# Kernel optimization log

Hardware: AMD Instinct MI355X
Metric: run time of the kernel (lower is better)

## Reference

```python
import jax, jax.numpy as jnp
import numpy as np

# ---- static config (LCNN wirenet) ----
K = 128            # fixed junction count per type (n_dyn_junc // n_type)
N_PTS0 = 32
N_PTS1 = 8
SCALE = N_PTS0 // N_PTS1   # maxpool1d kernel/stride = 4
DIM_LOI = 128
DIM_FC = 1024
FEATURE_DIM = 8
USE_COOD = 0.0
USE_SLOP = 0.0
HW = 128
B = 2
# static u<v pair indices (torch: meshgrid -> c = u < v), P = K*(K-1)/2
IU_np, IV_np = np.triu_indices(K, k=1)
P = IU_np.shape[0]
IU = jnp.asarray(IU_np, jnp.int32)
IV = jnp.asarray(IV_np, jnp.int32)
LAMBDA = jnp.linspace(0.0, 1.0, N_PTS0)[:, None]  # [32,1]


def setup_inputs() -> dict:
    key = jax.random.key(0)
    ks = jax.random.split(key, 8)
    inputs = jax.random.normal(ks[0], (B, 5, HW, HW), jnp.float32)
    features = jax.random.normal(ks[1], (B, 256, HW, HW), jnp.float32)
    fc1_w = jax.random.normal(ks[2], (DIM_LOI, 256), jnp.float32) * 0.05
    fc1_b = jnp.zeros((DIM_LOI,), jnp.float32)
    d_in = DIM_LOI * N_PTS1 + FEATURE_DIM  # 1032
    w1 = jax.random.normal(ks[3], (d_in, DIM_FC), jnp.float32) * 0.03
    b1 = jnp.zeros((DIM_FC,), jnp.float32)
    w2 = jax.random.normal(ks[4], (DIM_FC, DIM_FC), jnp.float32) * 0.03
    b2 = jnp.zeros((DIM_FC,), jnp.float32)
    w3 = jax.random.normal(ks[5], (DIM_FC, 1), jnp.float32) * 0.03
    b3 = jnp.zeros((1,), jnp.float32)
    return dict(inputs=inputs, features=features, fc1_w=fc1_w, fc1_b=fc1_b,
                w1=w1, b1=b1, w2=w2, b2=b2, w3=w3, b3=b3)


def _nms(a):
    # a: [1,H,W]; 3x3 max-pool NMS, keep only local maxima
    ap = jax.lax.reduce_window(a, -jnp.inf, jax.lax.max, (1, 3, 3), (1, 1, 1), 'SAME')
    return a * (a == ap).astype(a.dtype)


def _sample_lines(jmap, joff):
    # jmap: [1,H,W], joff: [1,2,H,W]  (inference path: dummy junc/Lpos)
    n_type = 1
    jm = _nms(jmap).reshape(n_type, -1)            # [1, HW*HW]
    jo = joff.reshape(n_type, 2, -1)
    score, index = jax.lax.top_k(jm, K)            # [1,K]
    y = (index // HW).astype(jnp.float32) + jnp.take_along_axis(jo[:, 0], index, 1) + 0.5
    x = (index % HW).astype(jnp.float32) + jnp.take_along_axis(jo[:, 1], index, 1) + 0.5
    xy = jnp.stack([y, x], -1)                     # [1,K,2]
    # inference dummies: junc=zeros(1,2), jtyp=zeros(1), Lpos=zeros(2,2)
    junc = jnp.zeros((1, 2), jnp.float32)
    jtyp = jnp.zeros((1,), jnp.int32)
    dist = jnp.sum((xy[:, :, None, :] - junc) ** 2, -1)  # [1,K,1]
    cost = jnp.min(dist, -1)
    match = jnp.argmin(dist, -1).astype(jnp.int32)       # [1,K]
    Njunc = 1
    match = jnp.where(jtyp[match] != jnp.arange(n_type, dtype=jnp.int32)[:, None], Njunc, match)
    match = jnp.where(cost > 1.5 * 1.5, Njunc, match).reshape(-1)  # [K]
    up, vp = match[IU], match[IV]
    Lpos = jnp.zeros((2, 2), jnp.float32)
    label = Lpos[up, vp]                           # [P]
    xyf = xy.reshape(n_type * K, 2)
    xyu, xyv = xyf[IU], xyf[IV]                    # [P,2]
    u2v = xyu - xyv
    u2v = u2v / jnp.clip(jnp.sqrt(jnp.sum(u2v ** 2, -1, keepdims=True)), 1e-6)
    feat = jnp.concatenate([
        xyu / HW * USE_COOD, xyv / HW * USE_COOD, u2v * USE_SLOP,
        (IU[:, None] > K).astype(jnp.float32), (IV[:, None] > K).astype(jnp.float32)], 1)  # [P,8]
    line = jnp.stack([xyu, xyv], 1)                # [P,2,2]
    return line, label, feat


def _loi_pool(xfeat, line):
    # xfeat: [C,H,W], line: [P,2,2] -> [P,C,N_PTS1]
    p = line[:, 0:1, :] * LAMBDA + line[:, 1:2, :] * (1.0 - LAMBDA) - 0.5  # [P,32,2]
    p = p.reshape(-1, 2)
    px, py = p[:, 0], p[:, 1]
    px0 = jnp.clip(jnp.floor(px), 0, HW - 1)
    py0 = jnp.clip(jnp.floor(py), 0, HW - 1)
    px1 = jnp.clip(px0 + 1, 0, HW - 1)
    py1 = jnp.clip(py0 + 1, 0, HW - 1)
    px0l = px0.astype(jnp.int32); py0l = py0.astype(jnp.int32)
    px1l = px1.astype(jnp.int32); py1l = py1.astype(jnp.int32)
    xp = (xfeat[:, px0l, py0l] * (px1 - px) * (py1 - py)
          + xfeat[:, px1l, py0l] * (px - px0) * (py1 - py)
          + xfeat[:, px0l, py1l] * (px1 - px) * (py - py0)
          + xfeat[:, px1l, py1l] * (px - px0) * (py - py0))  # [C, P*32]
    xp = xp.reshape(DIM_LOI, -1, N_PTS0).transpose(1, 0, 2)  # [P,C,32]
    # MaxPool1d(kernel=4, stride=4)
    return xp.reshape(xp.shape[0], DIM_LOI, N_PTS1, SCALE).max(-1)  # [P,C,8]


def _forward(inputs, features, fc1_w, fc1_b, w1, b1, w2, b2, w3, b3):
    b, _, r, c = inputs.shape
    out = jnp.transpose(inputs, (1, 0, 2, 3))       # [5,B,H,W]
    jmap_logits = out[0:2].reshape(1, 2, b, r, c)
    joff_logits = out[3:5].reshape(1, 2, b, r, c)
    jmap = jax.nn.softmax(jnp.transpose(jmap_logits, (2, 0, 1, 3, 4)), axis=2)[:, :, 1]  # [B,1,H,W]
    joff = jax.nn.sigmoid(jnp.transpose(joff_logits, (2, 0, 1, 3, 4))) - 0.5             # [B,1,2,H,W]
    # fc1: 1x1 conv 256 -> dim_loi
    xf = jnp.einsum('bchw,dc->bdhw', features, fc1_w) + fc1_b[None, :, None, None]
    lines, labels, feats = jax.vmap(_sample_lines)(jmap, joff)   # [B,P,2,2],[B,P],[B,P,8]
    # sample_lines runs under torch.no_grad()
    lines = jax.lax.stop_gradient(lines)
    labels = jax.lax.stop_gradient(labels)
    feats = jax.lax.stop_gradient(feats)
    xp = jax.vmap(_loi_pool)(xf, lines)             # [B,P,C,8]
    xv = xp.reshape(-1, N_PTS1 * DIM_LOI)           # [B*P, 1024] (C-major then pts)
    xv = jnp.concatenate([xv, feats.reshape(-1, FEATURE_DIM)], 1)  # [B*P, 1032]
    h = jax.nn.relu(xv @ w1 + b1)
    h = jax.nn.relu(h @ w2 + b2)
    scores = (h @ w3 + b3).reshape(-1)              # [B*P]
    return scores, labels.reshape(-1), lines


def reference(inputs, features, fc1_w, fc1_b, w1, b1, w2, b2, w3, b3):
    return _forward(inputs, features, fc1_w, fc1_b, w1, b1, w2, b2, w3, b3)
```

## Files before the change

kernel.cpp:

```cpp
#include <hip/hip_runtime.h>
#include <hip/hip_bf16.h>
#include <math.h>

#define HW 128
#define NPIX 16384
#define KTOP 128
#define PPAIR 8128
#define NB 2
#define DIMLOI 128
#define NROWS (NB*PPAIR)
#define MPAD 16384

typedef __bf16 bf16x8 __attribute__((ext_vector_type(8)));
typedef __bf16 bf16x4 __attribute__((ext_vector_type(4)));
typedef float floatx4 __attribute__((ext_vector_type(4)));

__device__ __forceinline__ unsigned long long mk_key(float v, int idx) {
    return ((unsigned long long)__float_as_uint(v) << 32) |
           (unsigned long long)(0xFFFFFFFFu - (unsigned)idx);
}

__device__ __forceinline__ unsigned long long shfl_xor_u64(unsigned long long x, int m) {
    unsigned lo = (unsigned)x, hi = (unsigned)(x >> 32);
    lo = __shfl_xor(lo, m);
    hi = __shfl_xor(hi, m);
    return ((unsigned long long)hi << 32) | lo;
}

__device__ __forceinline__ void bitonic_stage(unsigned long long V[4], int lane, int j, int k) {
    if (j >= 64) {
        int qm = j >> 6;
        #pragma unroll
        for (int q = 0; q < 4; q++) {
            int p = q ^ qm;
            if (p > q) {
                int i = q * 64 + lane;
                bool desc = ((i & k) == 0);
                unsigned long long a = V[q], b = V[p];
                unsigned long long hi = a > b ? a : b, lo = a > b ? b : a;
                V[q] = desc ? hi : lo;
                V[p] = desc ? lo : hi;
            }
        }
    } else {
        #pragma unroll
        for (int q = 0; q < 4; q++) {
            int i = q * 64 + lane;
            unsigned long long p = shfl_xor_u64(V[q], j);
            bool lower = (lane & j) == 0;
            bool desc = ((i & k) == 0);
            bool keepmax = (desc == lower);
            unsigned long long mx = V[q] > p ? V[q] : p;
            unsigned long long mn = V[q] > p ? p : V[q];
            V[q] = keepmax ? mx : mn;
        }
    }
}

__device__ __forceinline__ void sort256_desc(unsigned long long V[4], int lane) {
    #pragma unroll
    for (int k = 2; k <= 256; k <<= 1)
        #pragma unroll
        for (int j = k >> 1; j >= 1; j >>= 1)
            bitonic_stage(V, lane, j, k);
}

__device__ __forceinline__ void merge256_desc(unsigned long long V[4], int lane) {
    #pragma unroll
    for (int j = 128; j >= 1; j >>= 1)
        bitonic_stage(V, lane, j, 256);
}

__global__ __launch_bounds__(256) void nms_sort_kernel(const float* __restrict__ inp,
                                                       unsigned long long* __restrict__ tkeys) {
    __shared__ float jm[10 * HW];
    __shared__ unsigned long long cand[256];
    __shared__ int scnt;
    int blk = blockIdx.x;
    int b   = blockIdx.y;
    int tid = threadIdx.x, lane = tid & 63;
    int r0  = blk * 8;
    int rlo = (r0 > 0) ? r0 - 1 : 0;
    int rhi = (r0 + 8 < HW) ? r0 + 8 : HW - 1;
    int nrows = rhi - rlo + 1;

    for (int i = tid; i < nrows * HW; i += 256) {
        int pix = rlo * HW + i;
        float l0 = inp[((long)b * 5 + 0) * NPIX + pix];
        float l1 = inp[((long)b * 5 + 1) * NPIX + pix];
        float m = fmaxf(l0, l1);
        float e0 = expf(l0 - m), e1 = expf(l1 - m);
        jm[i] = e1 / (e0 + e1);
    }
    cand[tid] = 0ull;
    if (tid == 0) scnt = 0;
    __syncthreads();

    #pragma unroll
    for (int i = 0; i < 4; i++) {
        int pl = i * 256 + tid;
        int r = r0 + (pl >> 7), c = pl & 127;
        float v = jm[(r - rlo) * HW + c];
        float m = v;
        for (int dr = -1; dr <= 1; dr++) {
            int rr = r + dr;
            if (rr < 0 || rr >= HW) continue;
            for (int dc = -1; dc <= 1; dc++) {
                int cc = c + dc;
                if (cc < 0 || cc >= HW) continue;
                m = fmaxf(m, jm[(rr - rlo) * HW + cc]);
            }
        }
        float nv = (v == m) ? v : 0.f;
        bool has = (nv > 0.f);
        unsigned long long mask = __ballot(has);
        int n = __popcll(mask);
        int wbase = 0;
        if (lane == 0 && n) wbase = atomicAdd(&scnt, n);
        wbase = __shfl(wbase, 0);
        if (has) {
            int pos = wbase + __popcll(mask & ((1ull << lane) - 1ull));
            if (pos < 256) cand[pos] = mk_key(nv, r * HW + c);
        }
    }
    __syncthreads();
    if (blk == 0 && tid < 128 && tid >= scnt) cand[tid] = mk_key(0.f, tid);
    __syncthreads();

    if (tid < 64) {
        unsigned long long V[4];
        #pragma unroll
        for (int q = 0; q < 4; q++) V[q] = cand[q * 64 + lane];
        sort256_desc(V, lane);
        #pragma unroll
        for (int q = 0; q < 2; q++)
            tkeys[((long)b * 16 + blk) * 128 + q * 64 + lane] = V[q];
    }
}

__global__ __launch_bounds__(512) void topk_merge_kernel(const unsigned long long* __restrict__ tkeys,
                                                         const float* __restrict__ inp,
                                                         float* __restrict__ xy) {
    __shared__ unsigned long long Lb[16 * 128];
    __shared__ unsigned long long Mb[8 * 128];
    int b = blockIdx.x;
    int tid = threadIdx.x, w = tid >> 6, lane = tid & 63;
    for (int i = tid; i < 16 * 128; i += 512) Lb[i] = tkeys[(long)b * 2048 + i];
    __syncthreads();

    unsigned long long* src = Lb;
    unsigned long long* dst = Mb;
    for (int nact = 8; nact >= 1; nact >>= 1) {
        unsigned long long V[4];
        if (w < nact) {
            #pragma unroll
            for (int q = 0; q < 2; q++) V[q] = src[(2 * w) * 128 + q * 64 + lane];
            #pragma unroll
            for (int q = 2; q < 4; q++) {
                int t = (q - 2) * 64 + lane;
                V[q] = src[(2 * w + 1) * 128 + 127 - t];
            }
            merge256_desc(V, lane);
        }
        __syncthreads();
        if (w < nact) {
            #pragma unroll
            for (int q = 0; q < 2; q++) dst[w * 128 + q * 64 + lane] = V[q];
        }
        __syncthreads();
        unsigned long long* tmp = src; src = dst; dst = tmp;
    }

    if (tid < KTOP) {
        unsigned long long key = src[tid];
        int wi = (int)(0xFFFFFFFFu - (unsigned)(key & 0xFFFFFFFFull));
        int row = wi >> 7, col = wi & 127;
        float l3 = inp[((long)b * 5 + 3) * NPIX + wi];
        float l4 = inp[((long)b * 5 + 4) * NPIX + wi];
        float joy = 1.f / (1.f + expf(-l3)) - 0.5f;
        float jox = 1.f / (1.f + expf(-l4)) - 0.5f;
        xy[(b * KTOP + tid) * 2 + 0] = (float)row + joy + 0.5f;
        xy[(b * KTOP + tid) * 2 + 1] = (float)col + jox + 0.5f;
    }
}

__device__ __forceinline__ void pair_uv(int p, int& u, int& v) {
    int uu = (int)((255.0 - sqrt(65025.0 - 8.0 * (double)p)) * 0.5);
    if (uu < 0) uu = 0;
    while (uu * (255 - uu) / 2 > p) uu--;
    while ((uu + 1) * (255 - (uu + 1)) / 2 <= p) uu++;
    u = uu;
    v = uu + 1 + (p - uu * (255 - uu) / 2);
}

__global__ void lines_kernel(const float* __restrict__ xy, float* __restrict__ out) {
    int r = blockIdx.x * 256 + threadIdx.x;
    if (r >= NROWS) return;
    int b = r / PPAIR, p = r % PPAIR;
    int u, v; pair_uv(p, u, v);
    float yu = xy[(b * KTOP + u) * 2 + 0], xu = xy[(b * KTOP + u) * 2 + 1];
    float yv = xy[(b * KTOP + v) * 2 + 0], xv = xy[(b * KTOP + v) * 2 + 1];
    float* lines = out + 2 * NROWS;
    long base = (long)r * 4;
    lines[base + 0] = yu; lines[base + 1] = xu;
    lines[base + 2] = yv; lines[base + 3] = xv;
    out[NROWS + r] = 0.f;
}

__global__ void prep_weights(const float* __restrict__ w1, const float* __restrict__ w2,
                             const float* __restrict__ fc1w,
                             __hip_bfloat16* __restrict__ w1t, __hip_bfloat16* __restrict__ w2t,
                             __hip_bfloat16* __restrict__ fc1wb) {
    int z = blockIdx.z;
    int tx = threadIdx.x & 31, ty = threadIdx.x >> 5;
    if (z < 2) {
        const float* W = z ? w2 : w1;
        __hip_bfloat16* Wt = z ? w2t : w1t;
        __shared__ float t[32][33];
        int k0 = blockIdx.x * 32, n0 = blockIdx.y * 32;
        #pragma unroll
        for (int i = 0; i < 32; i += 8)
            t[ty + i][tx] = W[(long)(k0 + ty + i) * 1024 + n0 + tx];
        __syncthreads();
        #pragma unroll
        for (int i = 0; i < 32; i += 8)
            Wt[(long)(n0 + ty + i) * 1024 + k0 + tx] = __float2bfloat16(t[tx][ty + i]);
    } else {
        if (blockIdx.x < 4 && blockIdx.y < 8) {
            int r0 = blockIdx.x * 32, c0 = blockIdx.y * 32;
            #pragma unroll
            for (int i = 0; i < 32; i += 8) {
                long idx = (long)(r0 + ty + i) * 256 + c0 + tx;
                fc1wb[idx] = __float2bfloat16(fc1w[idx]);
            }
        }
    }
}

__device__ __forceinline__ void gload_lds16(const void* g, void* l) {
    __builtin_amdgcn_global_load_lds(
        (const __attribute__((address_space(1))) void*)g,
        (__attribute__((address_space(3))) void*)l, 16, 0, 0);
}

#define SA 264

__global__ __launch_bounds__(256) void xf_fused_kernel(
    const float* __restrict__ features, const __hip_bfloat16* __restrict__ fc1wb,
    const float* __restrict__ bias, __hip_bfloat16* __restrict__ C0) {
    __shared__ __align__(16) __bf16 A_lds[128 * SA];
    __shared__ __align__(16) unsigned short B_lds[128 * 32 * 8];
    int tid = threadIdx.x;
    int lane = tid & 63, wid = tid >> 6;
    int wr = wid >> 1, wc = wid & 1;
    int b = blockIdx.z;
    long pix0 = (long)blockIdx.x * 128;

    #pragma unroll
    for (int it = 0; it < 16; it++) {
        int slot = it * 256 + tid;
        int r = slot >> 5, s = slot & 31;
        int ss = s ^ (r & 7);
        gload_lds16(fc1wb + (size_t)r * 256 + ss * 8,
                    (char*)B_lds + (size_t)(it * 4096 + wid * 1024));
    }
    {
        int c = tid;
        const float* src = features + ((long)b * 256 + c) * NPIX + pix0;
        #pragma unroll
        for (int p4 = 0; p4 < 32; p4++) {
            floatx4 v = *(const floatx4*)(src + p4 * 4);
            #pragma unroll
            for (int e = 0; e < 4; e++)
                A_lds[(p4 * 4 + e) * SA + c] = (__bf16)v[e];
        }
    }
    __syncthreads();

    floatx4 acc[4][4];
    #pragma unroll
    for (int i = 0; i < 4; i++)
        #pragma unroll
        for (int j = 0; j < 4; j++) acc[i][j] = (floatx4){0.f, 0.f, 0.f, 0.f};

    int r15 = lane & 15;
    #pragma unroll
    for (int ks = 0; ks < 8; ks++) {
        int s = (lane >> 4) + ks * 4;
        bf16x8 af[4], bfr[4];
        #pragma unroll
        for (int mi = 0; mi < 4; mi++) {
            int R = wr * 64 + mi * 16 + r15;
            af[mi] = *(const bf16x8*)&A_lds[R * SA + s * 8];
        }
        #pragma unroll
        for (int ni = 0; ni < 4; ni++) {
            int Rn = wc * 64 + ni * 16 + r15;
            bfr[ni] = *(const bf16x8*)&B_lds[(size_t)Rn * 256 + ((s ^ (Rn & 7)) << 3)];
        }
        #pragma unroll
        for (int mi = 0; mi < 4; mi++)
            #pragma unroll
            for (int ni = 0; ni < 4; ni++)
                acc[mi][ni] = __builtin_amdgcn_mfma_f32_16x16x32_bf16(
                    af[mi], bfr[ni], acc[mi][ni], 0, 0, 0);
    }

    __hip_bfloat16* C = C0 + (long)b * NPIX * DIMLOI;
    #pragma unroll
    for (int ni = 0; ni < 4; ni++) {
        long c = wc * 64 + ni * 16 + r15;
        float bv = bias[c];
        #pragma unroll
        for (int mi = 0; mi < 4; mi++) {
            long rbase = pix0 + wr * 64 + mi * 16 + (lane >> 4) * 4;
            #pragma unroll
            for (int q = 0; q < 4; q++)
                C[(rbase + q) * (long)DIMLOI + c] = __float2bfloat16(acc[mi][ni][q] + bv);
        }
    }
}

#define BM 128
#define BN 128
#define BKK 64

template <bool SCORE>
__global__ __launch_bounds__(256) void gemm_mfma(
    const __hip_bfloat16* __restrict__ A, const __hip_bfloat16* __restrict__ Bt,
    const float* __restrict__ bias, __hip_bfloat16* __restrict__ C,
    int M, int N, int Kd,
    const float* __restrict__ w3, float* __restrict__ slab) {
    int bid = blockIdx.x;
    int xcd = bid & 7, j = bid >> 3;
    int mtpx = (M / BM) >> 3;
    int mt = xcd * mtpx + (j >> 3);
    int nt = j & 7;
    long row0 = (long)mt * BM, col0 = (long)nt * BN;

    __shared__ __align__(16) unsigned short As[BM * BKK];
    __shared__ __align__(16) unsigned short Bs[BN * BKK];
    int tid = threadIdx.x;
    int lane = tid & 63, wid = tid >> 6;
    int wr = wid >> 1, wc = wid & 1;

    floatx4 acc[4][4];
    #pragma unroll
    for (int i = 0; i < 4; i++)
        #pragma unroll
        for (int jj = 0; jj < 4; jj++) acc[i][jj] = (floatx4){0.f, 0.f, 0.f, 0.f};

    for (int k0 = 0; k0 < Kd; k0 += BKK) {
        #pragma unroll
        for (int it = 0; it < 4; it++) {
            int slot = wid * 256 + it * 64 + lane;
            int r = slot >> 3, s = slot & 7;
            int ss = s ^ (r & 7);
            gload_lds16(A + (row0 + r) * Kd + k0 + ss * 8,
                        (char*)As + (size_t)(wid * 4096 + it * 1024));
        }
        #pragma unroll
        for (int it = 0; it < 4; it++) {
            int slot = wid * 256 + it * 64 + lane;
            int r = slot >> 3, s = slot & 7;
            int ss = s ^ (r & 7);
            gload_lds16(Bt + (col0 + r) * Kd + k0 + ss * 8,
                        (char*)Bs + (size_t)(wid * 4096 + it * 1024));
        }
        __syncthreads();
        #pragma unroll
        for (int ks = 0; ks < 2; ks++) {
            bf16x8 af[4], bfr[4];
            int s = (lane >> 4) + ks * 4;
            #pragma unroll
            for (int mi = 0; mi < 4; mi++) {
                int R = wr * 64 + mi * 16 + (lane & 15);
                af[mi] = *(const bf16x8*)&As[R * BKK + ((s ^ (R & 7)) << 3)];
            }
            #pragma unroll
            for (int ni = 0; ni < 4; ni++) {
                int Rn = wc * 64 + ni * 16 + (lane & 15);
                bfr[ni] = *(const bf16x8*)&Bs[Rn * BKK + ((s ^ (Rn & 7)) << 3)];
            }
            #pragma unroll
            for (int mi = 0; mi < 4; mi++)
                #pragma unroll
                for (int ni = 0; ni < 4; ni++)
                    acc[mi][ni] = __builtin_amdgcn_mfma_f32_16x16x32_bf16(
                        af[mi], bfr[ni], acc[mi][ni], 0, 0, 0);
        }
        __syncthreads();
    }

    if constexpr (SCORE) {
        int ntile = (int)(col0 / BN);
        #pragma unroll
        for (int mi = 0; mi < 4; mi++) {
            #pragma unroll
            for (int q = 0; q < 4; q++) {
                float p = 0.f;
                #pragma unroll
                for (int ni = 0; ni < 4; ni++) {
                    long c = col0 + wc * 64 + ni * 16 + (lane & 15);
                    float v = fmaxf(acc[mi][ni][q] + bias[c], 0.f);
                    p += v * w3[c];
                }
                #pragma unroll
                for (int off = 1; off < 16; off <<= 1) p += __shfl_xor(p, off);
                if ((lane & 15) == 0) {
                    long row = row0 + wr * 64 + mi * 16 + (lane >> 4) * 4 + q;
                    slab[(long)(ntile * 2 + wc) * MPAD + row] = p;
                }
            }
        }
    } else {
        #pragma unroll
        for (int ni = 0; ni < 4; ni++) {
            long c = col0 + wc * 64 + ni * 16 + (lane & 15);
            float bv = bias[c];
            #pragma unroll
            for (int mi = 0; mi < 4; mi++) {
                long rbase = row0 + wr * 64 + mi * 16 + (lane >> 4) * 4;
                #pragma unroll
                for (int q = 0; q < 4; q++) {
                    float v = fmaxf(acc[mi][ni][q] + bv, 0.f);
                    C[(rbase + q) * (long)N + c] = __float2bfloat16(v);
                }
            }
        }
    }
}

__global__ void score_reduce_kernel(const float* __restrict__ slab, const float* __restrict__ b3,
                                    float* __restrict__ out) {
    int r = blockIdx.x * 256 + threadIdx.x;
    if (r >= NROWS) return;
    float s = b3[0];
    #pragma unroll
    for (int i = 0; i < 16; i++) s += slab[(long)i * MPAD + r];
    out[r] = s;
}

__global__ __launch_bounds__(256) void loi_sample_kernel(
    const __hip_bfloat16* __restrict__ xf, const float* __restrict__ xy,
    __hip_bfloat16* __restrict__ xp) {
    __shared__ int md[256 * 8];
    int tid = threadIdx.x;
    int sub = tid >> 5;
    int t   = tid & 31;
    int bid = blockIdx.x;
    int swz = (bid & 7) * 256 + (bid >> 3);
    int r   = swz * 8 + sub;
    int rm  = (r < NROWS) ? r : NROWS - 1;
    int b   = rm / PPAIR, p = rm % PPAIR;
    {
        int u, v; pair_uv(p, u, v);
        float yu = xy[(b * KTOP + u) * 2 + 0], xu = xy[(b * KTOP + u) * 2 + 1];
        float yv = xy[(b * KTOP + v) * 2 + 0], xv = xy[(b * KTOP + v) * 2 + 1];
        float lam = (float)t * (1.0f / 31.0f);
        float px = yu * lam + yv * (1.f - lam) - 0.5f;
        float py = xu * lam + xv * (1.f - lam) - 0.5f;
        float px0 = fminf(fmaxf(floorf(px), 0.f), 127.f);
        float py0 = fminf(fmaxf(floorf(py), 0.f), 127.f);
        float px1 = fminf(px0 + 1.f, 127.f);
        float py1 = fminf(py0 + 1.f, 127.f);
        int ix0 = (int)px0, iy0 = (int)py0, ix1 = (int)px1, iy1 = (int)py1;
        int base = tid * 8;
        md[base + 0] = (ix0 * HW + iy0) * (DIMLOI * 2);
        md[base + 1] = (ix1 * HW + iy0) * (DIMLOI * 2);
        md[base + 2] = (ix0 * HW + iy1) * (DIMLOI * 2);
        md[base + 3] = (ix1 * HW + iy1) * (DIMLOI * 2);
        md[base + 4] = __float_as_int((px1 - px) * (py1 - py));
        md[base + 5] = __float_as_int((px - px0) * (py1 - py));
        md[base + 6] = __float_as_int((px1 - px) * (py - py0));
        md[base + 7] = __float_as_int((px - px0) * (py - py0));
    }
    __syncthreads();

    const char* xfb = (const char*)(xf + (long)b * NPIX * DIMLOI) + t * 8;
    floatx4 mx[8];
    #pragma unroll
    for (int q = 0; q < 8; q++) mx[q] = (floatx4){-INFINITY, -INFINITY, -INFINITY, -INFINITY};
    #pragma unroll
    for (int tt = 0; tt < 32; tt++) {
        const int* m = &md[(sub * 32 + tt) * 8];
        bf16x4 v00 = *(const bf16x4*)(xfb + m[0]);
        bf16x4 v10 = *(const bf16x4*)(xfb + m[1]);
        bf16x4 v01 = *(const bf16x4*)(xfb + m[2]);
        bf16x4 v11 = *(const bf16x4*)(xfb + m[3]);
        float w00 = __int_as_float(m[4]), w10 = __int_as_float(m[5]);
        float w01 = __int_as_float(m[6]), w11 = __int_as_float(m[7]);
        floatx4 f00 = {(float)v00[0], (float)v00[1], (float)v00[2], (float)v00[3]};
        floatx4 f10 = {(float)v10[0], (float)v10[1], (float)v10[2], (float)v10[3]};
        floatx4 f01 = {(float)v01[0], (float)v01[1], (float)v01[2], (float)v01[3]};
        floatx4 f11 = {(float)v11[0], (float)v11[1], (float)v11[2], (float)v11[3]};
        floatx4 s = f00 * w00 + f10 * w10 + f01 * w01 + f11 * w11;
        mx[tt >> 2] = __builtin_elementwise_max(mx[tt >> 2], s);
    }
    __hip_bfloat16* rowp = xp + (long)r * 1024 + t * 32;
    #pragma unroll
    for (int e = 0; e < 4; e++) {
        bf16x8 o;
        #pragma unroll
        for (int q = 0; q < 8; q++) o[q] = (__bf16)mx[q][e];
        *(bf16x8*)(rowp + e * 8) = o;
    }
}

extern "C" void kernel_launch(void* const* d_in, const int* in_sizes, int n_in,
                              void* d_out, int out_size, void* d_ws, size_t ws_size,
                              hipStream_t stream) {
    const float* inputs   = (const float*)d_in[0];
    const float* features = (const float*)d_in[1];
    const float* fc1_w    = (const float*)d_in[2];
    const float* fc1_b    = (const float*)d_in[3];
    const float* w1       = (const float*)d_in[4];
    const float* b1       = (const float*)d_in[5];
    const float* w2       = (const float*)d_in[6];
    const float* b2       = (const float*)d_in[7];
    const float* w3       = (const float*)d_in[8];
    const float* b3       = (const float*)d_in[9];
    float* out = (float*)d_out;
    float* ws  = (float*)d_ws;

    float* xy   = ws + 65536;
    __hip_bfloat16* xfb16 = (__hip_bfloat16*)(ws + 66048);
    __hip_bfloat16* xp    = (__hip_bfloat16*)(ws + 4260352);
    __hip_bfloat16* h1    = (__hip_bfloat16*)(ws + 12648960);
    float* slab           = ws + 21037568;
    __hip_bfloat16* w1t   = (__hip_bfloat16*)(ws + 21299712);
    __hip_bfloat16* w2t   = (__hip_bfloat16*)(ws + 21824000);
    __hip_bfloat16* fc1wb = (__hip_bfloat16*)(ws + 22348288);
    unsigned long long* tkeys = (unsigned long long*)(ws + 22364672);

    prep_weights<<<dim3(32, 32, 3), 256, 0, stream>>>(w1, w2, fc1_w, w1t, w2t, fc1wb);

    nms_sort_kernel<<<dim3(16, NB), 256, 0, stream>>>(inputs, tkeys);
    topk_merge_kernel<<<NB, 512, 0, stream>>>(tkeys, inputs, xy);
    lines_kernel<<<(NROWS + 255) / 256, 256, 0, stream>>>(xy, out);

    xf_fused_kernel<<<dim3(NPIX / 128, 1, NB), 256, 0, stream>>>(
        features, fc1wb, fc1_b, xfb16);

    loi_sample_kernel<<<MPAD / 8, 256, 0, stream>>>(xfb16, xy, xp);

    gemm_mfma<false><<<(MPAD / BM) * 8, 256, 0, stream>>>(
        xp, w1t, b1, h1, MPAD, 1024, 1024, nullptr, nullptr);
    gemm_mfma<true><<<(MPAD / BM) * 8, 256, 0, stream>>>(
        h1, w2t, b2, nullptr, MPAD, 1024, 1024, w3, slab);
    score_reduce_kernel<<<(NROWS + 255) / 256, 256, 0, stream>>>(slab, b3, out);
}
```

Baseline: 176.3 us.

## Retile MLP GEMMs to 256x128 tiles with 32x32x16 MFMA and k-slot LDS layout

The two MLP GEMMs now use 256x128 block tiles instead of 128x128, switching from 16x16x32 to 32x32x16 bf16 MFMA instructions with 4x2 accumulator tiles per wave. The LDS layout changes from XOR-swizzled rows to a k-slot-major layout, which keeps LDS fragment reads contiguous. The intent is more reuse of each B tile, fewer LDS reads per MFMA and fewer instructions overall. The tradeoff is more accumulator registers, half as many blocks (launch_bounds 256,2), and a possible hit on global coalescing, since each lane now loads a different row.

```diff
diff --git a/kernel.cpp b/kernel.cpp
--- a/kernel.cpp
+++ b/kernel.cpp
@@ -14,6 +14,7 @@
 typedef __bf16 bf16x8 __attribute__((ext_vector_type(8)));
 typedef __bf16 bf16x4 __attribute__((ext_vector_type(4)));
 typedef float floatx4 __attribute__((ext_vector_type(4)));
+typedef float floatx16 __attribute__((ext_vector_type(16)));
 
 __device__ __forceinline__ unsigned long long mk_key(float v, int idx) {
     return ((unsigned long long)__float_as_uint(v) << 32) |
@@ -321,110 +322,103 @@
     }
 }
 
-#define BM 128
+#define BM 256
 #define BN 128
 #define BKK 64
 
 template <bool SCORE>
-__global__ __launch_bounds__(256) void gemm_mfma(
+__global__ __launch_bounds__(256, 2) void gemm_mlp(
     const __hip_bfloat16* __restrict__ A, const __hip_bfloat16* __restrict__ Bt,
     const float* __restrict__ bias, __hip_bfloat16* __restrict__ C,
-    int M, int N, int Kd,
     const float* __restrict__ w3, float* __restrict__ slab) {
+    __shared__ __align__(16) unsigned short As[8 * 256 * 8];
+    __shared__ __align__(16) unsigned short Bs[8 * 128 * 8];
+    int tid = threadIdx.x;
+    int lane = tid & 63, wid = tid >> 6;
+    int wr = wid >> 1, wn = wid & 1;
+    int r31 = lane & 31, khalf = lane >> 5;
     int bid = blockIdx.x;
     int xcd = bid & 7, j = bid >> 3;
-    int mtpx = (M / BM) >> 3;
-    int mt = xcd * mtpx + (j >> 3);
-    int nt = j & 7;
+    int mt = xcd * 8 + (j >> 3), nt = j & 7;
     long row0 = (long)mt * BM, col0 = (long)nt * BN;
 
-    __shared__ __align__(16) unsigned short As[BM * BKK];
-    __shared__ __align__(16) unsigned short Bs[BN * BKK];
-    int tid = threadIdx.x;
-    int lane = tid & 63, wid = tid >> 6;
-    int wr = wid >> 1, wc = wid & 1;
-
-    floatx4 acc[4][4];
-    #pragma unroll
-    for (int i = 0; i < 4; i++)
-        #pragma unroll
-        for (int jj = 0; jj < 4; jj++) acc[i][jj] = (floatx4){0.f, 0.f, 0.f, 0.f};
-
-    for (int k0 = 0; k0 < Kd; k0 += BKK) {
+    floatx16 acc[4][2];
+    #pragma unroll
+    for (int mi = 0; mi < 4; mi++)
+        #pragma unroll
+        for (int ni = 0; ni < 2; ni++)
+            #pragma unroll
+            for (int q = 0; q < 16; q++) acc[mi][ni][q] = 0.f;
+
+    for (int k0 = 0; k0 < 1024; k0 += BKK) {
+        #pragma unroll
+        for (int it = 0; it < 8; it++) {
+            int slot = it * 256 + tid;
+            int row = slot & 255, s = slot >> 8;
+            gload_lds16(A + (row0 + row) * 1024 + k0 + s * 8,
+                        (char*)As + (size_t)slot * 16 - (size_t)(lane * 16) + (size_t)(lane * 16));
+        }
         #pragma unroll
         for (int it = 0; it < 4; it++) {
-            int slot = wid * 256 + it * 64 + lane;
-            int r = slot >> 3, s = slot & 7;
-            int ss = s ^ (r & 7);
-            gload_lds16(A + (row0 + r) * Kd + k0 + ss * 8,
-                        (char*)As + (size_t)(wid * 4096 + it * 1024));
-        }
-        #pragma unroll
-        for (int it = 0; it < 4; it++) {
-            int slot = wid * 256 + it * 64 + lane;
-            int r = slot >> 3, s = slot & 7;
-            int ss = s ^ (r & 7);
-            gload_lds16(Bt + (col0 + r) * Kd + k0 + ss * 8,
-                        (char*)Bs + (size_t)(wid * 4096 + it * 1024));
+            int slot = it * 256 + tid;
+            int row = slot & 127, s = slot >> 7;
+            gload_lds16(Bt + (col0 + row) * 1024 + k0 + s * 8,
+                        (char*)Bs + (size_t)slot * 16 - (size_t)(lane * 16) + (size_t)(lane * 16));
         }
         __syncthreads();
         #pragma unroll
-        for (int ks = 0; ks < 2; ks++) {
-            bf16x8 af[4], bfr[4];
-            int s = (lane >> 4) + ks * 4;
-            #pragma unroll
-            for (int mi = 0; mi < 4; mi++) {
-                int R = wr * 64 + mi * 16 + (lane & 15);
-                af[mi] = *(const bf16x8*)&As[R * BKK + ((s ^ (R & 7)) << 3)];
-            }
-            #pragma unroll
-            for (int ni = 0; ni < 4; ni++) {
-                int Rn = wc * 64 + ni * 16 + (lane & 15);
-                bfr[ni] = *(const bf16x8*)&Bs[Rn * BKK + ((s ^ (Rn & 7)) << 3)];
-            }
+        for (int ks = 0; ks < 4; ks++) {
+            int kslot = ks * 2 + khalf;
+            bf16x8 af[4], bfr[2];
+            #pragma unroll
+            for (int mi = 0; mi < 4; mi++)
+                af[mi] = *(const bf16x8*)&As[(size_t)(kslot * 256 + wr * 128 + mi * 32 + r31) * 8];
+            #pragma unroll
+            for (int ni = 0; ni < 2; ni++)
+                bfr[ni] = *(const bf16x8*)&Bs[(size_t)(kslot * 128 + wn * 64 + ni * 32 + r31) * 8];
             #pragma unroll
             for (int mi = 0; mi < 4; mi++)
                 #pragma unroll
-                for (int ni = 0; ni < 4; ni++)
-                    acc[mi][ni] = __builtin_amdgcn_mfma_f32_16x16x32_bf16(
+                for (int ni = 0; ni < 2; ni++)
+                    acc[mi][ni] = __builtin_amdgcn_mfma_f32_32x32x16_bf16(
                         af[mi], bfr[ni], acc[mi][ni], 0, 0, 0);
         }
         __syncthreads();
     }
 
     if constexpr (SCORE) {
-        int ntile = (int)(col0 / BN);
+        int slot = nt * 2 + wn;
         #pragma unroll
         for (int mi = 0; mi < 4; mi++) {
             #pragma unroll
-            for (int q = 0; q < 4; q++) {
+            for (int q = 0; q < 16; q++) {
                 float p = 0.f;
                 #pragma unroll
-                for (int ni = 0; ni < 4; ni++) {
-                    long c = col0 + wc * 64 + ni * 16 + (lane & 15);
+                for (int ni = 0; ni < 2; ni++) {
+                    long c = col0 + wn * 64 + ni * 32 + r31;
                     float v = fmaxf(acc[mi][ni][q] + bias[c], 0.f);
                     p += v * w3[c];
                 }
                 #pragma unroll
-                for (int off = 1; off < 16; off <<= 1) p += __shfl_xor(p, off);
-                if ((lane & 15) == 0) {
-                    long row = row0 + wr * 64 + mi * 16 + (lane >> 4) * 4 + q;
-                    slab[(long)(ntile * 2 + wc) * MPAD + row] = p;
+                for (int off = 1; off < 32; off <<= 1) p += __shfl_xor(p, off);
+                if (r31 == 0) {
+                    long row = row0 + wr * 128 + mi * 32 + (q & 3) + 8 * (q >> 2) + 4 * khalf;
+                    slab[(long)slot * MPAD + row] = p;
                 }
             }
         }
     } else {
         #pragma unroll
-        for (int ni = 0; ni < 4; ni++) {
-            long c = col0 + wc * 64 + ni * 16 + (lane & 15);
-            float bv = bias[c];
-            #pragma unroll
-            for (int mi = 0; mi < 4; mi++) {
-                long rbase = row0 + wr * 64 + mi * 16 + (lane >> 4) * 4;
+        for (int mi = 0; mi < 4; mi++) {
+            #pragma unroll
+            for (int ni = 0; ni < 2; ni++) {
+                long c = col0 + wn * 64 + ni * 32 + r31;
+                float bv = bias[c];
                 #pragma unroll
-                for (int q = 0; q < 4; q++) {
+                for (int q = 0; q < 16; q++) {
+                    long row = row0 + wr * 128 + mi * 32 + (q & 3) + 8 * (q >> 2) + 4 * khalf;
                     float v = fmaxf(acc[mi][ni][q] + bv, 0.f);
-                    C[(rbase + q) * (long)N + c] = __float2bfloat16(v);
+                    C[row * 1024L + c] = __float2bfloat16(v);
                 }
             }
         }
@@ -544,9 +538,7 @@
 
     loi_sample_kernel<<<MPAD / 8, 256, 0, stream>>>(xfb16, xy, xp);
 
-    gemm_mfma<false><<<(MPAD / BM) * 8, 256, 0, stream>>>(
-        xp, w1t, b1, h1, MPAD, 1024, 1024, nullptr, nullptr);
-    gemm_mfma<true><<<(MPAD / BM) * 8, 256, 0, stream>>>(
-        h1, w2t, b2, nullptr, MPAD, 1024, 1024, w3, slab);
+    gemm_mlp<false><<<512, 256, 0, stream>>>(xp, w1t, b1, h1, nullptr, nullptr);
+    gemm_mlp<true><<<512, 256, 0, stream>>>(h1, w2t, b2, nullptr, w3, slab);
     score_reduce_kernel<<<(NROWS + 255) / 256, 256, 0, stream>>>(slab, b3, out);
 }
```

After: 234.9 us. +33.2%, slower.
